# Optimization experiments

Measured on AMD Instinct MI355X. Metric: run time of the kernel, lower is better.

The kernel has to match this reference:

```python
import jax, jax.numpy as jnp
import numpy as np

N = 20000   # nodes (ROIs, scaled up)
F = 20      # node_feat_dim
D = 256     # hidden_dim
H = 8       # heads
DK = D // H # 32
L = 3       # layers
S = 4       # sleep stages
E = 320000  # edges per stage


def _ln(x, g, b):
    mu = x.mean(-1, keepdims=True)
    v = ((x - mu) ** 2).mean(-1, keepdims=True)
    return (x - mu) / jnp.sqrt(v + 1e-5) * g + b


def setup_inputs() -> dict:
    key = jax.random.key(0)
    ks = jax.random.split(key, 16)
    rn = lambda k, s, sc=0.02: jax.random.normal(k, s, jnp.float32) * sc
    return {
        "x": jax.random.normal(ks[0], (N, F), jnp.float32),
        "edge_index": jax.random.randint(ks[1], (S, 2, E), 0, N, jnp.int32),
        "sc_mask": jax.random.randint(ks[2], (S, E), 0, 2, jnp.int32),
        "fc_weights": jax.random.normal(ks[3], (S, E), jnp.float32),
        "in_w": rn(ks[4], (F, D)), "in_b": jnp.zeros((D,), jnp.float32),
        "stage_emb": rn(ks[5], (S, D)),
        "Wq": rn(ks[6], (L, D, D)), "Wk": rn(ks[7], (L, D, D)),
        "Wv": rn(ks[8], (L, D, D)),
        "Wo": rn(ks[9], (L, D, D)), "bo": jnp.zeros((L, D), jnp.float32),
        "ln1_g": jnp.ones((L, D), jnp.float32), "ln1_b": jnp.zeros((L, D), jnp.float32),
        "ln2_g": jnp.ones((L, D), jnp.float32), "ln2_b": jnp.zeros((L, D), jnp.float32),
        "ffn_w1": rn(ks[10], (L, D, 4 * D)), "ffn_b1": jnp.zeros((L, 4 * D), jnp.float32),
        "ffn_w2": rn(ks[11], (L, 4 * D, D)), "ffn_b2": jnp.zeros((L, D), jnp.float32),
        "lam": jnp.full((L,), 0.5, jnp.float32),
        "fus_w": rn(ks[12], (S * D, D)), "fus_b": jnp.zeros((D,), jnp.float32),
        "out_g": jnp.ones((D,), jnp.float32), "out_b": jnp.zeros((D,), jnp.float32),
    }


def reference(x, edge_index, sc_mask, fc_weights, in_w, in_b, stage_emb,
              Wq, Wk, Wv, Wo, bo, ln1_g, ln1_b, ln2_g, ln2_b,
              ffn_w1, ffn_b1, ffn_w2, ffn_b2, lam, fus_w, fus_b, out_g, out_b):
    scale = DK ** 0.5
    stage_outs = []
    for k in range(S):  # fixed small stage count
        src, dst = edge_index[k, 0], edge_index[k, 1]
        sc = sc_mask[k].astype(jnp.float32)
        fcw = fc_weights[k]
        h = x @ in_w + in_b + stage_emb[k]
        for l in range(L):  # fixed small layer count
            Q = (h @ Wq[l]).reshape(N, H, DK)
            K = (h @ Wk[l]).reshape(N, H, DK)
            V = (h @ Wv[l]).reshape(N, H, DK)
            # edge-wise gathered dot-product scores  [E, H]
            attn = (Q[dst] * K[src]).sum(-1) / scale
            attn = attn * sc[:, None] + lam[l] * fcw[:, None]
            # segment softmax grouped by destination node (PyG softmax)
            m = jax.ops.segment_max(attn, dst, num_segments=N)
            e = jnp.exp(attn - m[dst])
            s = jax.ops.segment_sum(e, dst, num_segments=N)
            a = e / (s[dst] + 1e-16)
            # scatter-add weighted V_j  [N, H, DK]
            agg = jax.ops.segment_sum(a[:, :, None] * V[src], dst, num_segments=N)
            out = agg.reshape(N, D) @ Wo[l] + bo[l]
            out = _ln(out + h, ln1_g[l], ln1_b[l])  # residual_proj is Identity (in==out)
            f = jax.nn.gelu(out @ ffn_w1[l] + ffn_b1[l], approximate=False)
            f = f @ ffn_w2[l] + ffn_b2[l]
            h = _ln(out + f, ln2_g[l], ln2_b[l])
        stage_outs.append(h)
    h_concat = jnp.concatenate(stage_outs, axis=-1)  # [N, S*D]
    return _ln(h_concat @ fus_w + fus_b, out_g, out_b)
```

## Files before the change

### kernel.cpp

```cpp
#include <hip/hip_runtime.h>
#include <hip/hip_bf16.h>
#include <math.h>

#define N_NODES 20000
#define FDIM 20
#define DDIM 256
#define HH 8
#define LL 3
#define SS 4
#define EE 320000

typedef __attribute__((ext_vector_type(8))) short bf16x8;
typedef __attribute__((ext_vector_type(8))) unsigned short u16x8;
typedef __attribute__((ext_vector_type(4))) float f32x4;

__device__ inline unsigned short f2bf(float f) {
  unsigned u = __float_as_uint(f);
  unsigned r = u + 0x7FFFu + ((u >> 16) & 1u);
  return (unsigned short)(r >> 16);
}
__device__ inline float bf2f(unsigned short u) {
  return __uint_as_float(((unsigned)u) << 16);
}

__global__ __launch_bounds__(256) void gemm_f32_kernel(
    const float* __restrict__ A, const float* __restrict__ B,
    const float* __restrict__ bias, float* __restrict__ C,
    int M, int Nc, int K)
{
  __shared__ float As[16][65];
  __shared__ float Bs[16][65];
  const int tid = threadIdx.x;
  const int tx = tid & 15, ty = tid >> 4;
  const int row0 = blockIdx.y * 64, col0 = blockIdx.x * 64;
  const int am = tid >> 2, ak = (tid & 3) * 4;
  const int bk = tid >> 4, bc = (tid & 15) * 4;
  float acc[4][4] = {};
  for (int k0 = 0; k0 < K; k0 += 16) {
    float4 av = make_float4(0.f, 0.f, 0.f, 0.f);
    int garow = row0 + am;
    if (garow < M) {
      if (k0 + ak + 3 < K) {
        av = *(const float4*)(A + (size_t)garow * K + k0 + ak);
      } else {
        float t[4];
        #pragma unroll
        for (int j = 0; j < 4; j++)
          t[j] = (k0 + ak + j < K) ? A[(size_t)garow * K + k0 + ak + j] : 0.f;
        av = make_float4(t[0], t[1], t[2], t[3]);
      }
    }
    As[ak + 0][am] = av.x; As[ak + 1][am] = av.y;
    As[ak + 2][am] = av.z; As[ak + 3][am] = av.w;
    float4 bv = make_float4(0.f, 0.f, 0.f, 0.f);
    if (k0 + bk < K)
      bv = *(const float4*)(B + (size_t)(k0 + bk) * Nc + col0 + bc);
    Bs[bk][bc + 0] = bv.x; Bs[bk][bc + 1] = bv.y;
    Bs[bk][bc + 2] = bv.z; Bs[bk][bc + 3] = bv.w;
    __syncthreads();
    #pragma unroll
    for (int kk = 0; kk < 16; kk++) {
      float a[4], b[4];
      #pragma unroll
      for (int i = 0; i < 4; i++) a[i] = As[kk][ty * 4 + i];
      #pragma unroll
      for (int j = 0; j < 4; j++) b[j] = Bs[kk][tx * 4 + j];
      #pragma unroll
      for (int i = 0; i < 4; i++)
        #pragma unroll
        for (int j = 0; j < 4; j++)
          acc[i][j] = fmaf(a[i], b[j], acc[i][j]);
    }
    __syncthreads();
  }
  #pragma unroll
  for (int i = 0; i < 4; i++) {
    int row = row0 + ty * 4 + i;
    if (row >= M) continue;
    int col = col0 + tx * 4;
    float4 v;
    float* vp = &v.x;
    #pragma unroll
    for (int j = 0; j < 4; j++) vp[j] = acc[i][j] + bias[col + j];
    *(float4*)(C + (size_t)row * Nc + col) = v;
  }
}

template<int ACT>
__global__ __launch_bounds__(256) void mfma_gemm64(
    const unsigned short* __restrict__ A, const unsigned short* __restrict__ BT,
    const float* __restrict__ bias, unsigned short* __restrict__ Cb,
    int ldc, int M, int K, int ldb)
{
  __shared__ unsigned short As[64][40];
  __shared__ unsigned short Bs[128][40];
  const int tid = threadIdx.x, lane = tid & 63, wid = tid >> 6;
  const int wr = (wid >> 1) * 32, wc = (wid & 1) * 64;
  const int row0 = blockIdx.y * 64, col0 = blockIdx.x * 128;
  const int sr = tid >> 2, sc = (tid & 3) * 8;
  f32x4 acc[2][4] = {};
  for (int k0 = 0; k0 < K; k0 += 32) {
    {
      int gr = row0 + sr;
      u16x8 av = {0,0,0,0,0,0,0,0};
      if (gr < M) av = *(const u16x8*)(A + (size_t)gr * K + k0 + sc);
      *(u16x8*)&As[sr][sc] = av;
    }
    #pragma unroll
    for (int p = 0; p < 2; p++) {
      int n = p * 64 + sr;
      u16x8 bv = *(const u16x8*)(BT + (size_t)(col0 + n) * ldb + k0 + sc);
      *(u16x8*)&Bs[n][sc] = bv;
    }
    __syncthreads();
    bf16x8 af[2], bfv[4];
    #pragma unroll
    for (int mi = 0; mi < 2; mi++)
      af[mi] = *(const bf16x8*)&As[wr + mi * 16 + (lane & 15)][(lane >> 4) * 8];
    #pragma unroll
    for (int ni = 0; ni < 4; ni++)
      bfv[ni] = *(const bf16x8*)&Bs[wc + ni * 16 + (lane & 15)][(lane >> 4) * 8];
    #pragma unroll
    for (int mi = 0; mi < 2; mi++)
      #pragma unroll
      for (int ni = 0; ni < 4; ni++)
        acc[mi][ni] = __builtin_amdgcn_mfma_f32_16x16x32_bf16(af[mi], bfv[ni], acc[mi][ni], 0, 0, 0);
    __syncthreads();
  }
  #pragma unroll
  for (int mi = 0; mi < 2; mi++) {
    #pragma unroll
    for (int ni = 0; ni < 4; ni++) {
      int col = col0 + wc + ni * 16 + (lane & 15);
      float bval = bias ? bias[col] : 0.f;
      #pragma unroll
      for (int j = 0; j < 4; j++) {
        int row = row0 + wr + mi * 16 + (lane >> 4) * 4 + j;
        if (row < M) {
          float t = acc[mi][ni][j] + bval;
          if (ACT == 1) t = 0.5f * t * (1.f + erff(t * 0.7071067811865475f));
          Cb[(size_t)row * ldc + col] = f2bf(t);
        }
      }
    }
  }
}

template<int KTILES, int DO_LN, int ACCUM>
__global__ __launch_bounds__(256) void gemm_ln_kernel(
    const unsigned short* __restrict__ A, const unsigned short* __restrict__ BT,
    const float* __restrict__ bias, const float* __restrict__ resid,
    const float* __restrict__ gv, const float* __restrict__ bv,
    float* __restrict__ outf, unsigned short* __restrict__ outb,
    int M, int ldb, int bk0)
{
  constexpr int K = KTILES * 32;
  __shared__ unsigned short As[32][40];
  __shared__ unsigned short Bs[256][40];
  __shared__ float red[32][4][2];
  __shared__ float stats[32][2];
  const int tid = threadIdx.x, lane = tid & 63, w = tid >> 6;
  const int row0 = blockIdx.x * 32;
  const int sr2 = tid >> 3, sc2 = (tid & 7) * 4;
  const int sr = tid >> 2, sc = (tid & 3) * 8;
  const int g16 = lane >> 4, c15 = lane & 15;
  f32x4 acc[2][4] = {};
  for (int kt = 0; kt < KTILES; kt++) {
    int k0 = kt * 32;
    {
      int gr = row0 + sr2;
      ushort4 av = make_ushort4(0, 0, 0, 0);
      if (gr < M) av = *(const ushort4*)(A + (size_t)gr * K + k0 + sc2);
      *(ushort4*)&As[sr2][sc2] = av;
    }
    #pragma unroll
    for (int p = 0; p < 4; p++) {
      int n = p * 64 + sr;
      u16x8 bv8 = *(const u16x8*)(BT + (size_t)n * ldb + bk0 + k0 + sc);
      *(u16x8*)&Bs[n][sc] = bv8;
    }
    __syncthreads();
    bf16x8 af[2], bfv[4];
    #pragma unroll
    for (int mi = 0; mi < 2; mi++)
      af[mi] = *(const bf16x8*)&As[mi * 16 + c15][g16 * 8];
    #pragma unroll
    for (int ni = 0; ni < 4; ni++)
      bfv[ni] = *(const bf16x8*)&Bs[w * 64 + ni * 16 + c15][g16 * 8];
    #pragma unroll
    for (int mi = 0; mi < 2; mi++)
      #pragma unroll
      for (int ni = 0; ni < 4; ni++)
        acc[mi][ni] = __builtin_amdgcn_mfma_f32_16x16x32_bf16(af[mi], bfv[ni], acc[mi][ni], 0, 0, 0);
    __syncthreads();
  }
  #pragma unroll
  for (int mi = 0; mi < 2; mi++)
    #pragma unroll
    for (int ni = 0; ni < 4; ni++) {
      int col = w * 64 + ni * 16 + c15;
      float bval = bias ? bias[col] : 0.f;
      #pragma unroll
      for (int j = 0; j < 4; j++) {
        int row = row0 + mi * 16 + g16 * 4 + j;
        float t = acc[mi][ni][j] + bval;
        if (row < M) {
          if (DO_LN) t += resid[(size_t)row * DDIM + col];
          if (ACCUM) t += outf[(size_t)row * DDIM + col];
        }
        acc[mi][ni][j] = t;
      }
    }
  if (DO_LN) {
    #pragma unroll
    for (int mi = 0; mi < 2; mi++)
      #pragma unroll
      for (int j = 0; j < 4; j++) {
        float s = 0.f, q = 0.f;
        #pragma unroll
        for (int ni = 0; ni < 4; ni++) { float t = acc[mi][ni][j]; s += t; q += t * t; }
        #pragma unroll
        for (int d = 1; d < 16; d <<= 1) { s += __shfl_xor(s, d); q += __shfl_xor(q, d); }
        if (c15 == 0) {
          int r = mi * 16 + g16 * 4 + j;
          red[r][w][0] = s; red[r][w][1] = q;
        }
      }
    __syncthreads();
    if (tid < 32) {
      float s = red[tid][0][0] + red[tid][1][0] + red[tid][2][0] + red[tid][3][0];
      float q = red[tid][0][1] + red[tid][1][1] + red[tid][2][1] + red[tid][3][1];
      float mu = s * (1.f / DDIM);
      float var = q * (1.f / DDIM) - mu * mu;
      stats[tid][0] = mu;
      stats[tid][1] = rsqrtf(var + 1e-5f);
    }
    __syncthreads();
  }
  #pragma unroll
  for (int mi = 0; mi < 2; mi++)
    #pragma unroll
    for (int ni = 0; ni < 4; ni++) {
      int col = w * 64 + ni * 16 + c15;
      #pragma unroll
      for (int j = 0; j < 4; j++) {
        int r = mi * 16 + g16 * 4 + j;
        int row = row0 + r;
        if (row >= M) continue;
        float t = acc[mi][ni][j];
        float o = DO_LN ? (t - stats[r][0]) * stats[r][1] * gv[col] + bv[col] : t;
        outf[(size_t)row * DDIM + col] = o;
        if (DO_LN) outb[(size_t)row * DDIM + col] = f2bf(o);
      }
    }
}

__global__ __launch_bounds__(256) void transpose_bf16_tiled(
    const float* __restrict__ W, unsigned short* __restrict__ WT,
    int K, int Nn, int ldo, size_t istr, size_t ostr)
{
  __shared__ unsigned short t[64][65];
  const float* src = W + blockIdx.z * istr;
  unsigned short* dst = WT + blockIdx.z * ostr;
  int tid = threadIdx.x;
  int ty = tid >> 4, tx = tid & 15;
  int k0 = blockIdx.y * 64, n0 = blockIdx.x * 64;
  #pragma unroll
  for (int r = 0; r < 4; r++) {
    int k = k0 + r * 16 + ty;
    float4 v = *(const float4*)(src + (size_t)k * Nn + n0 + tx * 4);
    t[tx * 4 + 0][r * 16 + ty] = f2bf(v.x);
    t[tx * 4 + 1][r * 16 + ty] = f2bf(v.y);
    t[tx * 4 + 2][r * 16 + ty] = f2bf(v.z);
    t[tx * 4 + 3][r * 16 + ty] = f2bf(v.w);
  }
  __syncthreads();
  #pragma unroll
  for (int r = 0; r < 4; r++) {
    int n = r * 16 + ty;
    ushort4 o;
    o.x = t[n][tx * 4 + 0]; o.y = t[n][tx * 4 + 1];
    o.z = t[n][tx * 4 + 2]; o.w = t[n][tx * 4 + 3];
    *(ushort4*)(dst + (size_t)(n0 + n) * ldo + k0 + tx * 4) = o;
  }
}

__global__ void ifill_kernel(int* __restrict__ p, int v, int n) {
  int i = blockIdx.x * blockDim.x + threadIdx.x;
  if (i < n) p[i] = v;
}

__global__ void add_emb_dual(const float* __restrict__ base, const float* __restrict__ se,
                             float* __restrict__ h, unsigned short* __restrict__ hb) {
  int i4 = blockIdx.x * blockDim.x + threadIdx.x;
  if (i4 >= N_NODES * 64) return;
  float4 v = ((const float4*)base)[i4];
  float4 e = ((const float4*)se)[i4 & 63];
  v.x += e.x; v.y += e.y; v.z += e.z; v.w += e.w;
  ((float4*)h)[i4] = v;
  ushort4 o;
  o.x = f2bf(v.x); o.y = f2bf(v.y); o.z = f2bf(v.z); o.w = f2bf(v.w);
  ((ushort4*)hb)[i4] = o;
}

__global__ void hist_kernel(const int* __restrict__ dst, int* __restrict__ deg) {
  int e = blockIdx.x * blockDim.x + threadIdx.x;
  if (e < EE) atomicAdd(&deg[dst[e]], 1);
}

__global__ __launch_bounds__(1024) void scan_kernel(const int* __restrict__ deg,
                                                    int* __restrict__ rowptr) {
  __shared__ int part[1024];
  const int t = threadIdx.x;
  const int CH = (N_NODES + 1023) / 1024;
  int base = t * CH, s = 0;
  for (int i = 0; i < CH; i++) {
    int idx = base + i;
    if (idx < N_NODES) s += deg[idx];
  }
  part[t] = s;
  __syncthreads();
  for (int off = 1; off < 1024; off <<= 1) {
    int v = (t >= off) ? part[t - off] : 0;
    __syncthreads();
    part[t] += v;
    __syncthreads();
  }
  int run = (t == 0) ? 0 : part[t - 1];
  for (int i = 0; i < CH; i++) {
    int idx = base + i;
    if (idx < N_NODES) { rowptr[idx] = run; run += deg[idx]; }
  }
  if (t == 1023) rowptr[N_NODES] = run;
}

__global__ void csrfill_kernel(const int* __restrict__ src, const int* __restrict__ dst,
                               const int* __restrict__ scm, const float* __restrict__ fcw,
                               const int* __restrict__ rowptr, int* __restrict__ cur,
                               int2* __restrict__ epe) {
  int e = blockIdx.x * blockDim.x + threadIdx.x;
  if (e >= EE) return;
  int d = dst[e];
  int slot = rowptr[d] + atomicAdd(&cur[d], 1);
  epe[slot] = make_int2(src[e] | (scm[e] << 31), __float_as_int(fcw[e]));
}

__global__ __launch_bounds__(256) void attn_agg_kernel(
    const unsigned short* __restrict__ QKV,
    const int* __restrict__ rowptr, const int2* __restrict__ epe,
    const float* __restrict__ lam, int l,
    unsigned short* __restrict__ agg)
{
  int node = blockIdx.x * 4 + (threadIdx.x >> 6);
  int lane = threadIdx.x & 63;
  if (node >= N_NODES) return;
  const float laml = lam[l];
  ushort4 q4 = *(const ushort4*)(QKV + (size_t)node * 768 + lane * 4);
  float qx = bf2f(q4.x), qy = bf2f(q4.y), qz = bf2f(q4.z), qw = bf2f(q4.w);
  int beg = rowptr[node], end = rowptr[node + 1];
  float m = -INFINITY, ss = 0.f;
  float ax = 0.f, ay = 0.f, az = 0.f, aw = 0.f;
  int i = beg;
  for (; i + 1 < end; i += 2) {
    int2 ea = epe[i], eb = epe[i + 1];
    int sa = ea.x & 0x7FFFFFFF, sb = eb.x & 0x7FFFFFFF;
    float sca = (float)(((unsigned)ea.x) >> 31);
    float scb = (float)(((unsigned)eb.x) >> 31);
    float fwa = __int_as_float(ea.y), fwb = __int_as_float(eb.y);
    const unsigned short* kpa = QKV + (size_t)sa * 768 + 256 + lane * 4;
    const unsigned short* kpb = QKV + (size_t)sb * 768 + 256 + lane * 4;
    ushort4 ka = *(const ushort4*)kpa;
    ushort4 va = *(const ushort4*)(kpa + 256);
    ushort4 kb = *(const ushort4*)kpb;
    ushort4 vb = *(const ushort4*)(kpb + 256);
    float da = qx * bf2f(ka.x) + qy * bf2f(ka.y) + qz * bf2f(ka.z) + qw * bf2f(ka.w);
    float db = qx * bf2f(kb.x) + qy * bf2f(kb.y) + qz * bf2f(kb.z) + qw * bf2f(kb.w);
    da += __shfl_xor(da, 1); db += __shfl_xor(db, 1);
    da += __shfl_xor(da, 2); db += __shfl_xor(db, 2);
    da += __shfl_xor(da, 4); db += __shfl_xor(db, 4);
    float s0 = da * 0.17677669529663687f * sca + laml * fwa;
    float s1 = db * 0.17677669529663687f * scb + laml * fwb;
    float mn = fmaxf(m, fmaxf(s0, s1));
    float corr = __expf(m - mn);
    float p0 = __expf(s0 - mn);
    float p1 = __expf(s1 - mn);
    ss = ss * corr + p0 + p1;
    ax = ax * corr + p0 * bf2f(va.x) + p1 * bf2f(vb.x);
    ay = ay * corr + p0 * bf2f(va.y) + p1 * bf2f(vb.y);
    az = az * corr + p0 * bf2f(va.z) + p1 * bf2f(vb.z);
    aw = aw * corr + p0 * bf2f(va.w) + p1 * bf2f(vb.w);
    m = mn;
  }
  if (i < end) {
    int2 ea = epe[i];
    int sa = ea.x & 0x7FFFFFFF;
    float sca = (float)(((unsigned)ea.x) >> 31);
    float fwa = __int_as_float(ea.y);
    const unsigned short* kpa = QKV + (size_t)sa * 768 + 256 + lane * 4;
    ushort4 ka = *(const ushort4*)kpa;
    ushort4 va = *(const ushort4*)(kpa + 256);
    float da = qx * bf2f(ka.x) + qy * bf2f(ka.y) + qz * bf2f(ka.z) + qw * bf2f(ka.w);
    da += __shfl_xor(da, 1);
    da += __shfl_xor(da, 2);
    da += __shfl_xor(da, 4);
    float s0 = da * 0.17677669529663687f * sca + laml * fwa;
    float mn = fmaxf(m, s0);
    float corr = __expf(m - mn);
    float p0 = __expf(s0 - mn);
    ss = ss * corr + p0;
    ax = ax * corr + p0 * bf2f(va.x);
    ay = ay * corr + p0 * bf2f(va.y);
    az = az * corr + p0 * bf2f(va.z);
    aw = aw * corr + p0 * bf2f(va.w);
    m = mn;
  }
  float inv = 1.f / (ss + 1e-16f);
  ushort4 o;
  o.x = f2bf(ax * inv); o.y = f2bf(ay * inv);
  o.z = f2bf(az * inv); o.w = f2bf(aw * inv);
  *(ushort4*)(agg + (size_t)node * DDIM + lane * 4) = o;
}

__global__ __launch_bounds__(256) void ln_kernel(
    const float* __restrict__ X, const float* __restrict__ g,
    const float* __restrict__ b, float* __restrict__ out, int M)
{
  int row = blockIdx.x * (blockDim.x >> 6) + (threadIdx.x >> 6);
  int lane = threadIdx.x & 63;
  if (row >= M) return;
  float4 x = ((const float4*)(X + (size_t)row * DDIM))[lane];
  float s = x.x + x.y + x.z + x.w;
  #pragma unroll
  for (int mk = 1; mk < 64; mk <<= 1) s += __shfl_xor(s, mk);
  float mu = s * (1.f / DDIM);
  float d0 = x.x - mu, d1 = x.y - mu, d2 = x.z - mu, d3 = x.w - mu;
  float vs = d0 * d0 + d1 * d1 + d2 * d2 + d3 * d3;
  #pragma unroll
  for (int mk = 1; mk < 64; mk <<= 1) vs += __shfl_xor(vs, mk);
  float inv = rsqrtf(vs * (1.f / DDIM) + 1e-5f);
  float4 gg = ((const float4*)g)[lane];
  float4 bb = ((const float4*)b)[lane];
  float4 o;
  o.x = d0 * inv * gg.x + bb.x;
  o.y = d1 * inv * gg.y + bb.y;
  o.z = d2 * inv * gg.z + bb.z;
  o.w = d3 * inv * gg.w + bb.w;
  ((float4*)(out + (size_t)row * DDIM))[lane] = o;
}

extern "C" void kernel_launch(void* const* d_in, const int* in_sizes, int n_in,
                              void* d_out, int out_size, void* d_ws, size_t ws_size,
                              hipStream_t stream) {
  const float* x      = (const float*)d_in[0];
  const int*   ei     = (const int*)d_in[1];
  const int*   scm    = (const int*)d_in[2];
  const float* fcw    = (const float*)d_in[3];
  const float* in_w   = (const float*)d_in[4];
  const float* in_b   = (const float*)d_in[5];
  const float* st_emb = (const float*)d_in[6];
  const float* Wq     = (const float*)d_in[7];
  const float* Wk     = (const float*)d_in[8];
  const float* Wv     = (const float*)d_in[9];
  const float* Wo     = (const float*)d_in[10];
  const float* bo     = (const float*)d_in[11];
  const float* ln1g   = (const float*)d_in[12];
  const float* ln1b   = (const float*)d_in[13];
  const float* ln2g   = (const float*)d_in[14];
  const float* ln2b   = (const float*)d_in[15];
  const float* fw1    = (const float*)d_in[16];
  const float* fb1    = (const float*)d_in[17];
  const float* fw2    = (const float*)d_in[18];
  const float* fb2    = (const float*)d_in[19];
  const float* lam    = (const float*)d_in[20];
  const float* fus_w  = (const float*)d_in[21];
  const float* fus_b  = (const float*)d_in[22];
  const float* outg   = (const float*)d_in[23];
  const float* outb   = (const float*)d_in[24];

  const size_t ND = (size_t)N_NODES * DDIM;
  const int DD = DDIM * DDIM;
  float* W = (float*)d_ws;
  size_t off = 0;
  auto alloc = [&](size_t n) { float* p = W + off; off += n; return p; };
  float* u1 = alloc((size_t)N_NODES * 1024 / 2);
  unsigned short* f1  = (unsigned short*)u1;
  unsigned short* QKV = (unsigned short*)u1;
  unsigned short* aggb    = (unsigned short*)alloc(ND / 2);
  float* base = alloc(ND);
  float* h    = alloc(ND);
  float* out1 = alloc(ND);
  unsigned short* h_bf    = (unsigned short*)alloc(ND / 2);
  unsigned short* out1_bf = (unsigned short*)alloc(ND / 2);
  unsigned short* bfb = (unsigned short*)alloc(1310720);
  unsigned short* wqkvT = bfb;
  unsigned short* woT   = bfb + 589824;
  unsigned short* fw1T  = bfb + 786432;
  unsigned short* fw2T  = bfb + 1572864;
  unsigned short* fusT  = bfb + 2359296;
  int*  rowptr = (int*)alloc(N_NODES + 4);
  int*  deg    = (int*)alloc(N_NODES);
  int*  cur    = (int*)alloc(N_NODES);
  int2* epe    = (int2*)alloc(EE * 2);
  float* fus   = (float*)d_out;

  transpose_bf16_tiled<<<dim3(4, 4, 3), 256, 0, stream>>>(Wq, wqkvT,           DDIM, DDIM, DDIM, DD, 196608);
  transpose_bf16_tiled<<<dim3(4, 4, 3), 256, 0, stream>>>(Wk, wqkvT + 65536,   DDIM, DDIM, DDIM, DD, 196608);
  transpose_bf16_tiled<<<dim3(4, 4, 3), 256, 0, stream>>>(Wv, wqkvT + 131072,  DDIM, DDIM, DDIM, DD, 196608);
  transpose_bf16_tiled<<<dim3(4, 4, 3), 256, 0, stream>>>(Wo, woT,             DDIM, DDIM, DDIM, DD, DD);
  transpose_bf16_tiled<<<dim3(16, 4, 3), 256, 0, stream>>>(fw1, fw1T, DDIM, 4 * DDIM, DDIM, 4 * DD, 4 * DD);
  transpose_bf16_tiled<<<dim3(4, 16, 3), 256, 0, stream>>>(fw2, fw2T, 4 * DDIM, DDIM, 4 * DDIM, 4 * DD, 4 * DD);
  transpose_bf16_tiled<<<dim3(4, 16, 1), 256, 0, stream>>>(fus_w, fusT, 4 * DDIM, DDIM, 4 * DDIM, 0, 0);

  dim3 gF32(DDIM / 64, (N_NODES + 63) / 64);
  gemm_f32_kernel<<<gF32, 256, 0, stream>>>(x, in_w, in_b, base, N_NODES, DDIM, FDIM);

  const int eBlocks  = (EE + 255) / 256;
  const int n2Blocks = (2 * N_NODES + 255) / 256;
  const int lnBlocks = (N_NODES + 3) / 4;
  const int emBlocks = (N_NODES * 64 + 255) / 256;
  dim3 gQKV(6, (N_NODES + 63) / 64);
  dim3 gFFN1(8, (N_NODES + 63) / 64);
  const int fusedBlocks = (N_NODES + 31) / 32;

  for (int s = 0; s < SS; s++) {
    const int* srcp = ei + (size_t)s * 2 * EE;
    const int* dstp = srcp + EE;
    const int* scs  = scm + (size_t)s * EE;
    const float* fcs = fcw + (size_t)s * EE;

    ifill_kernel<<<n2Blocks, 256, 0, stream>>>(deg, 0, 2 * N_NODES);
    hist_kernel<<<eBlocks, 256, 0, stream>>>(dstp, deg);
    scan_kernel<<<1, 1024, 0, stream>>>(deg, rowptr);
    csrfill_kernel<<<eBlocks, 256, 0, stream>>>(srcp, dstp, scs, fcs, rowptr, cur, epe);

    add_emb_dual<<<emBlocks, 256, 0, stream>>>(base, st_emb + s * DDIM, h, h_bf);

    for (int l = 0; l < LL; l++) {
      mfma_gemm64<0><<<gQKV, 256, 0, stream>>>(
          h_bf, wqkvT + (size_t)l * 196608, nullptr, QKV, 768, N_NODES, DDIM, DDIM);

      attn_agg_kernel<<<lnBlocks, 256, 0, stream>>>(QKV, rowptr, epe, lam, l, aggb);

      gemm_ln_kernel<8, 1, 0><<<fusedBlocks, 256, 0, stream>>>(
          aggb, woT + (size_t)l * DD, bo + l * DDIM, h,
          ln1g + l * DDIM, ln1b + l * DDIM, out1, out1_bf, N_NODES, DDIM, 0);

      mfma_gemm64<1><<<gFFN1, 256, 0, stream>>>(
          out1_bf, fw1T + (size_t)l * 4 * DD, fb1 + l * 4 * DDIM, f1, 4 * DDIM,
          N_NODES, DDIM, DDIM);

      gemm_ln_kernel<32, 1, 0><<<fusedBlocks, 256, 0, stream>>>(
          f1, fw2T + (size_t)l * 4 * DD, fb2 + l * DDIM, out1,
          ln2g + l * DDIM, ln2b + l * DDIM, h, h_bf, N_NODES, 4 * DDIM, 0);
    }

    if (s == 0)
      gemm_ln_kernel<8, 0, 0><<<fusedBlocks, 256, 0, stream>>>(
          h_bf, fusT, fus_b, nullptr, nullptr, nullptr, fus, nullptr,
          N_NODES, 4 * DDIM, s * DDIM);
    else
      gemm_ln_kernel<8, 0, 1><<<fusedBlocks, 256, 0, stream>>>(
          h_bf, fusT, nullptr, nullptr, nullptr, nullptr, fus, nullptr,
          N_NODES, 4 * DDIM, s * DDIM);
  }

  ln_kernel<<<lnBlocks, 256, 0, stream>>>(fus, outg, outb, (float*)d_out, N_NODES);
}
```

Baseline: 2.684 ms.

## Load GEMM fragments directly from global memory and unroll attention gather by four

Both MFMA GEMM kernels drop the shared-memory staging and the per-tile barriers. Each lane now loads its bf16x8 A and B fragments straight from global memory, with the K loop unrolled by four so loads from several iterations can be in flight at once. Data reuse now depends on L1/L2 caching rather than LDS, so global load traffic goes up. Separately, the edge attention loop handles four edges per iteration instead of two, giving more outstanding gathers of K and V rows.

```diff
diff --git a/kernel.cpp b/kernel.cpp
--- a/kernel.cpp
+++ b/kernel.cpp
@@ -87,55 +87,49 @@
 }
 
 template<int ACT>
-__global__ __launch_bounds__(256) void mfma_gemm64(
+__global__ __launch_bounds__(256) void mfma_gemm_direct(
     const unsigned short* __restrict__ A, const unsigned short* __restrict__ BT,
     const float* __restrict__ bias, unsigned short* __restrict__ Cb,
     int ldc, int M, int K, int ldb)
 {
-  __shared__ unsigned short As[64][40];
-  __shared__ unsigned short Bs[128][40];
   const int tid = threadIdx.x, lane = tid & 63, wid = tid >> 6;
   const int wr = (wid >> 1) * 32, wc = (wid & 1) * 64;
   const int row0 = blockIdx.y * 64, col0 = blockIdx.x * 128;
-  const int sr = tid >> 2, sc = (tid & 3) * 8;
+  const int c15 = lane & 15, g16 = lane >> 4;
   f32x4 acc[2][4] = {};
+  const unsigned short* Ap[2];
+  #pragma unroll
+  for (int mi = 0; mi < 2; mi++) {
+    int r = row0 + wr + mi * 16 + c15;
+    if (r > M - 1) r = M - 1;
+    Ap[mi] = A + (size_t)r * K + g16 * 8;
+  }
+  const unsigned short* Bp[4];
+  #pragma unroll
+  for (int ni = 0; ni < 4; ni++)
+    Bp[ni] = BT + (size_t)(col0 + wc + ni * 16 + c15) * ldb + g16 * 8;
+  #pragma unroll 4
   for (int k0 = 0; k0 < K; k0 += 32) {
-    {
-      int gr = row0 + sr;
-      u16x8 av = {0,0,0,0,0,0,0,0};
-      if (gr < M) av = *(const u16x8*)(A + (size_t)gr * K + k0 + sc);
-      *(u16x8*)&As[sr][sc] = av;
-    }
-    #pragma unroll
-    for (int p = 0; p < 2; p++) {
-      int n = p * 64 + sr;
-      u16x8 bv = *(const u16x8*)(BT + (size_t)(col0 + n) * ldb + k0 + sc);
-      *(u16x8*)&Bs[n][sc] = bv;
-    }
-    __syncthreads();
     bf16x8 af[2], bfv[4];
     #pragma unroll
-    for (int mi = 0; mi < 2; mi++)
-      af[mi] = *(const bf16x8*)&As[wr + mi * 16 + (lane & 15)][(lane >> 4) * 8];
-    #pragma unroll
-    for (int ni = 0; ni < 4; ni++)
-      bfv[ni] = *(const bf16x8*)&Bs[wc + ni * 16 + (lane & 15)][(lane >> 4) * 8];
+    for (int mi = 0; mi < 2; mi++) af[mi] = *(const bf16x8*)(Ap[mi] + k0);
+    #pragma unroll
+    for (int ni = 0; ni < 4; ni++) bfv[ni] = *(const bf16x8*)(Bp[ni] + k0);
     #pragma unroll
     for (int mi = 0; mi < 2; mi++)
       #pragma unroll
       for (int ni = 0; ni < 4; ni++)
         acc[mi][ni] = __builtin_amdgcn_mfma_f32_16x16x32_bf16(af[mi], bfv[ni], acc[mi][ni], 0, 0, 0);
-    __syncthreads();
   }
   #pragma unroll
   for (int mi = 0; mi < 2; mi++) {
     #pragma unroll
     for (int ni = 0; ni < 4; ni++) {
-      int col = col0 + wc + ni * 16 + (lane & 15);
+      int col = col0 + wc + ni * 16 + c15;
       float bval = bias ? bias[col] : 0.f;
       #pragma unroll
       for (int j = 0; j < 4; j++) {
-        int row = row0 + wr + mi * 16 + (lane >> 4) * 4 + j;
+        int row = row0 + wr + mi * 16 + g16 * 4 + j;
         if (row < M) {
           float t = acc[mi][ni][j] + bval;
           if (ACT == 1) t = 0.5f * t * (1.f + erff(t * 0.7071067811865475f));
@@ -147,7 +141,7 @@
 }
 
 template<int KTILES, int DO_LN, int ACCUM>
-__global__ __launch_bounds__(256) void gemm_ln_kernel(
+__global__ __launch_bounds__(256) void gemm_ln_direct(
     const unsigned short* __restrict__ A, const unsigned short* __restrict__ BT,
     const float* __restrict__ bias, const float* __restrict__ resid,
     const float* __restrict__ gv, const float* __restrict__ bv,
@@ -155,44 +149,36 @@
     int M, int ldb, int bk0)
 {
   constexpr int K = KTILES * 32;
-  __shared__ unsigned short As[32][40];
-  __shared__ unsigned short Bs[256][40];
   __shared__ float red[32][4][2];
   __shared__ float stats[32][2];
   const int tid = threadIdx.x, lane = tid & 63, w = tid >> 6;
   const int row0 = blockIdx.x * 32;
-  const int sr2 = tid >> 3, sc2 = (tid & 7) * 4;
-  const int sr = tid >> 2, sc = (tid & 3) * 8;
-  const int g16 = lane >> 4, c15 = lane & 15;
+  const int c15 = lane & 15, g16 = lane >> 4;
   f32x4 acc[2][4] = {};
+  const unsigned short* Ap[2];
+  #pragma unroll
+  for (int mi = 0; mi < 2; mi++) {
+    int r = row0 + mi * 16 + c15;
+    if (r > M - 1) r = M - 1;
+    Ap[mi] = A + (size_t)r * K + g16 * 8;
+  }
+  const unsigned short* Bp[4];
+  #pragma unroll
+  for (int ni = 0; ni < 4; ni++)
+    Bp[ni] = BT + (size_t)(w * 64 + ni * 16 + c15) * ldb + bk0 + g16 * 8;
+  #pragma unroll 4
   for (int kt = 0; kt < KTILES; kt++) {
     int k0 = kt * 32;
-    {
-      int gr = row0 + sr2;
-      ushort4 av = make_ushort4(0, 0, 0, 0);
-      if (gr < M) av = *(const ushort4*)(A + (size_t)gr * K + k0 + sc2);
-      *(ushort4*)&As[sr2][sc2] = av;
-    }
-    #pragma unroll
-    for (int p = 0; p < 4; p++) {
-      int n = p * 64 + sr;
-      u16x8 bv8 = *(const u16x8*)(BT + (size_t)n * ldb + bk0 + k0 + sc);
-      *(u16x8*)&Bs[n][sc] = bv8;
-    }
-    __syncthreads();
     bf16x8 af[2], bfv[4];
     #pragma unroll
-    for (int mi = 0; mi < 2; mi++)
-      af[mi] = *(const bf16x8*)&As[mi * 16 + c15][g16 * 8];
-    #pragma unroll
-    for (int ni = 0; ni < 4; ni++)
-      bfv[ni] = *(const bf16x8*)&Bs[w * 64 + ni * 16 + c15][g16 * 8];
+    for (int mi = 0; mi < 2; mi++) af[mi] = *(const bf16x8*)(Ap[mi] + k0);
+    #pragma unroll
+    for (int ni = 0; ni < 4; ni++) bfv[ni] = *(const bf16x8*)(Bp[ni] + k0);
     #pragma unroll
     for (int mi = 0; mi < 2; mi++)
       #pragma unroll
       for (int ni = 0; ni < 4; ni++)
         acc[mi][ni] = __builtin_amdgcn_mfma_f32_16x16x32_bf16(af[mi], bfv[ni], acc[mi][ni], 0, 0, 0);
-    __syncthreads();
   }
   #pragma unroll
   for (int mi = 0; mi < 2; mi++)
@@ -361,49 +347,48 @@
   float m = -INFINITY, ss = 0.f;
   float ax = 0.f, ay = 0.f, az = 0.f, aw = 0.f;
   int i = beg;
-  for (; i + 1 < end; i += 2) {
-    int2 ea = epe[i], eb = epe[i + 1];
-    int sa = ea.x & 0x7FFFFFFF, sb = eb.x & 0x7FFFFFFF;
-    float sca = (float)(((unsigned)ea.x) >> 31);
-    float scb = (float)(((unsigned)eb.x) >> 31);
-    float fwa = __int_as_float(ea.y), fwb = __int_as_float(eb.y);
-    const unsigned short* kpa = QKV + (size_t)sa * 768 + 256 + lane * 4;
-    const unsigned short* kpb = QKV + (size_t)sb * 768 + 256 + lane * 4;
-    ushort4 ka = *(const ushort4*)kpa;
-    ushort4 va = *(const ushort4*)(kpa + 256);
-    ushort4 kb = *(const ushort4*)kpb;
-    ushort4 vb = *(const ushort4*)(kpb + 256);
-    float da = qx * bf2f(ka.x) + qy * bf2f(ka.y) + qz * bf2f(ka.z) + qw * bf2f(ka.w);
-    float db = qx * bf2f(kb.x) + qy * bf2f(kb.y) + qz * bf2f(kb.z) + qw * bf2f(kb.w);
-    da += __shfl_xor(da, 1); db += __shfl_xor(db, 1);
-    da += __shfl_xor(da, 2); db += __shfl_xor(db, 2);
-    da += __shfl_xor(da, 4); db += __shfl_xor(db, 4);
-    float s0 = da * 0.17677669529663687f * sca + laml * fwa;
-    float s1 = db * 0.17677669529663687f * scb + laml * fwb;
-    float mn = fmaxf(m, fmaxf(s0, s1));
+  for (; i + 3 < end; i += 4) {
+    int2 e0 = epe[i], e1 = epe[i + 1], e2 = epe[i + 2], e3 = epe[i + 3];
+    const unsigned short* kp0 = QKV + (size_t)(e0.x & 0x7FFFFFFF) * 768 + 256 + lane * 4;
+    const unsigned short* kp1 = QKV + (size_t)(e1.x & 0x7FFFFFFF) * 768 + 256 + lane * 4;
+    const unsigned short* kp2 = QKV + (size_t)(e2.x & 0x7FFFFFFF) * 768 + 256 + lane * 4;
+    const unsigned short* kp3 = QKV + (size_t)(e3.x & 0x7FFFFFFF) * 768 + 256 + lane * 4;
+    ushort4 k0 = *(const ushort4*)kp0, v0 = *(const ushort4*)(kp0 + 256);
+    ushort4 k1 = *(const ushort4*)kp1, v1 = *(const ushort4*)(kp1 + 256);
+    ushort4 k2 = *(const ushort4*)kp2, v2 = *(const ushort4*)(kp2 + 256);
+    ushort4 k3 = *(const ushort4*)kp3, v3 = *(const ushort4*)(kp3 + 256);
+    float d0 = qx * bf2f(k0.x) + qy * bf2f(k0.y) + qz * bf2f(k0.z) + qw * bf2f(k0.w);
+    float d1 = qx * bf2f(k1.x) + qy * bf2f(k1.y) + qz * bf2f(k1.z) + qw * bf2f(k1.w);
+    float d2 = qx * bf2f(k2.x) + qy * bf2f(k2.y) + qz * bf2f(k2.z) + qw * bf2f(k2.w);
+    float d3 = qx * bf2f(k3.x) + qy * bf2f(k3.y) + qz * bf2f(k3.z) + qw * bf2f(k3.w);
+    d0 += __shfl_xor(d0, 1); d1 += __shfl_xor(d1, 1); d2 += __shfl_xor(d2, 1); d3 += __shfl_xor(d3, 1);
+    d0 += __shfl_xor(d0, 2); d1 += __shfl_xor(d1, 2); d2 += __shfl_xor(d2, 2); d3 += __shfl_xor(d3, 2);
+    d0 += __shfl_xor(d0, 4); d1 += __shfl_xor(d1, 4); d2 += __shfl_xor(d2, 4); d3 += __shfl_xor(d3, 4);
+    float s0 = d0 * 0.17677669529663687f * (float)(((unsigned)e0.x) >> 31) + laml * __int_as_float(e0.y);
+    float s1 = d1 * 0.17677669529663687f * (float)(((unsigned)e1.x) >> 31) + laml * __int_as_float(e1.y);
+    float s2 = d2 * 0.17677669529663687f * (float)(((unsigned)e2.x) >> 31) + laml * __int_as_float(e2.y);
+    float s3 = d3 * 0.17677669529663687f * (float)(((unsigned)e3.x) >> 31) + laml * __int_as_float(e3.y);
+    float mn = fmaxf(fmaxf(m, fmaxf(s0, s1)), fmaxf(s2, s3));
     float corr = __expf(m - mn);
-    float p0 = __expf(s0 - mn);
-    float p1 = __expf(s1 - mn);
-    ss = ss * corr + p0 + p1;
-    ax = ax * corr + p0 * bf2f(va.x) + p1 * bf2f(vb.x);
-    ay = ay * corr + p0 * bf2f(va.y) + p1 * bf2f(vb.y);
-    az = az * corr + p0 * bf2f(va.z) + p1 * bf2f(vb.z);
-    aw = aw * corr + p0 * bf2f(va.w) + p1 * bf2f(vb.w);
+    float p0 = __expf(s0 - mn), p1 = __expf(s1 - mn);
+    float p2 = __expf(s2 - mn), p3 = __expf(s3 - mn);
+    ss = ss * corr + (p0 + p1) + (p2 + p3);
+    ax = ax * corr + p0 * bf2f(v0.x) + p1 * bf2f(v1.x) + p2 * bf2f(v2.x) + p3 * bf2f(v3.x);
+    ay = ay * corr + p0 * bf2f(v0.y) + p1 * bf2f(v1.y) + p2 * bf2f(v2.y) + p3 * bf2f(v3.y);
+    az = az * corr + p0 * bf2f(v0.z) + p1 * bf2f(v1.z) + p2 * bf2f(v2.z) + p3 * bf2f(v3.z);
+    aw = aw * corr + p0 * bf2f(v0.w) + p1 * bf2f(v1.w) + p2 * bf2f(v2.w) + p3 * bf2f(v3.w);
     m = mn;
   }
-  if (i < end) {
+  for (; i < end; i++) {
     int2 ea = epe[i];
-    int sa = ea.x & 0x7FFFFFFF;
-    float sca = (float)(((unsigned)ea.x) >> 31);
-    float fwa = __int_as_float(ea.y);
-    const unsigned short* kpa = QKV + (size_t)sa * 768 + 256 + lane * 4;
+    const unsigned short* kpa = QKV + (size_t)(ea.x & 0x7FFFFFFF) * 768 + 256 + lane * 4;
     ushort4 ka = *(const ushort4*)kpa;
     ushort4 va = *(const ushort4*)(kpa + 256);
     float da = qx * bf2f(ka.x) + qy * bf2f(ka.y) + qz * bf2f(ka.z) + qw * bf2f(ka.w);
     da += __shfl_xor(da, 1);
     da += __shfl_xor(da, 2);
     da += __shfl_xor(da, 4);
-    float s0 = da * 0.17677669529663687f * sca + laml * fwa;
+    float s0 = da * 0.17677669529663687f * (float)(((unsigned)ea.x) >> 31) + laml * __int_as_float(ea.y);
     float mn = fmaxf(m, s0);
     float corr = __expf(m - mn);
     float p0 = __expf(s0 - mn);
@@ -536,30 +521,30 @@
     add_emb_dual<<<emBlocks, 256, 0, stream>>>(base, st_emb + s * DDIM, h, h_bf);
 
     for (int l = 0; l < LL; l++) {
-      mfma_gemm64<0><<<gQKV, 256, 0, stream>>>(
+      mfma_gemm_direct<0><<<gQKV, 256, 0, stream>>>(
           h_bf, wqkvT + (size_t)l * 196608, nullptr, QKV, 768, N_NODES, DDIM, DDIM);
 
       attn_agg_kernel<<<lnBlocks, 256, 0, stream>>>(QKV, rowptr, epe, lam, l, aggb);
 
-      gemm_ln_kernel<8, 1, 0><<<fusedBlocks, 256, 0, stream>>>(
+      gemm_ln_direct<8, 1, 0><<<fusedBlocks, 256, 0, stream>>>(
           aggb, woT + (size_t)l * DD, bo + l * DDIM, h,
           ln1g + l * DDIM, ln1b + l * DDIM, out1, out1_bf, N_NODES, DDIM, 0);
 
-      mfma_gemm64<1><<<gFFN1, 256, 0, stream>>>(
+      mfma_gemm_direct<1><<<gFFN1, 256, 0, stream>>>(
           out1_bf, fw1T + (size_t)l * 4 * DD, fb1 + l * 4 * DDIM, f1, 4 * DDIM,
           N_NODES, DDIM, DDIM);
 
-      gemm_ln_kernel<32, 1, 0><<<fusedBlocks, 256, 0, stream>>>(
+      gemm_ln_direct<32, 1, 0><<<fusedBlocks, 256, 0, stream>>>(
           f1, fw2T + (size_t)l * 4 * DD, fb2 + l * DDIM, out1,
           ln2g + l * DDIM, ln2b + l * DDIM, h, h_bf, N_NODES, 4 * DDIM, 0);
     }
 
     if (s == 0)
-      gemm_ln_kernel<8, 0, 0><<<fusedBlocks, 256, 0, stream>>>(
+      gemm_ln_direct<8, 0, 0><<<fusedBlocks, 256, 0, stream>>>(
           h_bf, fusT, fus_b, nullptr, nullptr, nullptr, fus, nullptr,
           N_NODES, 4 * DDIM, s * DDIM);
     else
-      gemm_ln_kernel<8, 0, 1><<<fusedBlocks, 256, 0, stream>>>(
+      gemm_ln_direct<8, 0, 1><<<fusedBlocks, 256, 0, stream>>>(
           h_bf, fusT, nullptr, nullptr, nullptr, nullptr, fus, nullptr,
           N_NODES, 4 * DDIM, s * DDIM);
   }
```

Result: slower. 3.849 ms (+43.4%).
